# Kernel optimization log

Measured on AMD Instinct MI355X. Metric: run time of the kernel, lower is better.

The kernel has to match this reference:

```python
import jax, jax.numpy as jnp
import numpy as np

N = 50000
E = 800000
IN_C = 128
HID = 128
OUT_C = 128
EPS = 1e-5


def _glorot(key, shape):
    fan_in = shape[-1]
    return jax.random.normal(key, shape, dtype=jnp.float32) / jnp.sqrt(jnp.float32(fan_in))


def setup_inputs() -> dict:
    key = jax.random.key(0)
    ks = jax.random.split(key, 16)
    inp = {
        'x': jax.random.normal(ks[0], (N, IN_C), dtype=jnp.float32),
        'edge_index': jax.random.randint(ks[1], (2, E), 0, N, dtype=jnp.int64),
    }
    dims = [(IN_C, HID), (HID, HID), (HID, OUT_C)]
    for i, (din, dout) in enumerate(dims, start=1):
        inp[f'Wl{i}'] = _glorot(ks[2 * i], (dout, din))      # applied to aggregated neighbors
        inp[f'bl{i}'] = jnp.zeros((dout,), dtype=jnp.float32)
        inp[f'Wr{i}'] = _glorot(ks[2 * i + 1], (dout, din))  # applied to root node
        inp[f'g{i}'] = jnp.ones((dout,), dtype=jnp.float32)   # BN gamma
        inp[f'b{i}'] = jnp.zeros((dout,), dtype=jnp.float32)  # BN beta
    inp['Wlin'] = _glorot(ks[10], (OUT_C, 2 * HID + OUT_C))
    inp['blin'] = jnp.zeros((OUT_C,), dtype=jnp.float32)
    return inp


def _sage(x, src, dst, Wl, bl, Wr):
    # mean aggregation of source features at target nodes (PyG SAGEConv default)
    msg = x[src]                                              # [E, C]
    s = jax.ops.segment_sum(msg, dst, num_segments=N)         # [N, C]
    cnt = jax.ops.segment_sum(jnp.ones((src.shape[0], 1), x.dtype), dst, num_segments=N)
    aggr = s / jnp.maximum(cnt, 1.0)
    return aggr @ Wl.T + bl + x @ Wr.T


def _bn(x, g, b):
    # training-mode BatchNorm1d over the node dimension
    mu = jnp.mean(x, axis=0)
    var = jnp.var(x, axis=0)
    return g * (x - mu) * jax.lax.rsqrt(var + EPS) + b


def reference(x, edge_index, Wl1, bl1, Wr1, g1, b1, Wl2, bl2, Wr2, g2, b2,
              Wl3, bl3, Wr3, g3, b3, Wlin, blin):
    src, dst = edge_index[0], edge_index[1]
    x1 = _bn(jax.nn.relu(_sage(x, src, dst, Wl1, bl1, Wr1)), g1, b1)
    x2 = _bn(jax.nn.relu(_sage(x1, src, dst, Wl2, bl2, Wr2)), g2, b2)
    x3 = _bn(jax.nn.relu(_sage(x2, src, dst, Wl3, bl3, Wr3)), g3, b3)
    cat = jnp.concatenate([x1, x2, x3], axis=-1)              # [N, 2*HID + OUT_C]
    return jax.nn.relu(cat @ Wlin.T + blin)
```

## Files before the change

### kernel.cpp

```cpp
#include <hip/hip_runtime.h>

#define NN 50000
#define NE 800000
#define CH 128
#define EPSV 1e-5f
#define NPASS 2
#define PRANGE 25000
#define NBLK 49

typedef unsigned short ushort_t;
typedef __attribute__((ext_vector_type(8))) short short8_t;
typedef __attribute__((ext_vector_type(8))) unsigned short u16x8;
typedef __attribute__((ext_vector_type(4))) float f32x4;

#define AS1 __attribute__((address_space(1)))
#define AS3 __attribute__((address_space(3)))

__device__ inline float bf2f(ushort_t u) {
    union { unsigned int i; float f; } t; t.i = ((unsigned int)u) << 16; return t.f;
}
__device__ inline ushort_t f2bf(float f) {
    union { float f; unsigned int i; } t; t.f = f;
    unsigned int r = t.i + 0x7fff + ((t.i >> 16) & 1);
    return (ushort_t)(r >> 16);
}


__global__ void k_hist(const int* __restrict__ dst, int* __restrict__ deg) {
    int e = blockIdx.x * 256 + threadIdx.x;
    if (e < NE) atomicAdd(&deg[dst[e]], 1);
}

__global__ __launch_bounds__(1024) void k_scanA(const int* __restrict__ deg,
                                                int* __restrict__ rp,
                                                int* __restrict__ btot) {
    __shared__ int wsum[16];
    const int t = threadIdx.x;
    const int lane = t & 63;
    const int wid = t >> 6;
    const int i = blockIdx.x * 1024 + t;
    int v = (i < NN) ? deg[i] : 0;
    int x = v;
    #pragma unroll
    for (int off = 1; off < 64; off <<= 1) {
        int y = __shfl_up(x, off, 64);
        if (lane >= off) x += y;
    }
    if (lane == 63) wsum[wid] = x;
    __syncthreads();
    if (wid == 0 && lane < 16) {
        int s = wsum[lane];
        #pragma unroll
        for (int off = 1; off < 16; off <<= 1) {
            int y = __shfl_up(s, off, 16);
            if (lane >= off) s += y;
        }
        wsum[lane] = s;
    }
    __syncthreads();
    int wbase = (wid > 0) ? wsum[wid - 1] : 0;
    if (i < NN) rp[i] = wbase + x - v;
    if (wid == 15 && lane == 63) btot[blockIdx.x] = wbase + x;
}

__global__ void k_scanB(const int* __restrict__ btot, int* __restrict__ boffs,
                        int* __restrict__ rp) {
    int t = threadIdx.x;
    int v = (t < NBLK) ? btot[t] : 0;
    int x = v;
    #pragma unroll
    for (int off = 1; off < 64; off <<= 1) {
        int y = __shfl_up(x, off, 64);
        if (t >= off) x += y;
    }
    if (t < NBLK) boffs[t] = x - v;
    if (t == NBLK - 1) rp[NN] = x;
}

__global__ __launch_bounds__(256) void k_scanC(int* __restrict__ rp,
                                               const int* __restrict__ boffs) {
    int i = blockIdx.x * 256 + threadIdx.x;
    if (i < NN) rp[i] += boffs[i >> 10];
}

__global__ void k_fillp(const int* __restrict__ src, const int* __restrict__ dst,
                        const int* __restrict__ rp, int* __restrict__ cur,
                        int* __restrict__ csr, int lo, int hi) {
    int e = blockIdx.x * 256 + threadIdx.x;
    if (e < NE) {
        int d = dst[e];
        int s = src[e];
        if (d >= lo && d < hi) {
            int pos = rp[d] + atomicAdd(&cur[d], 1);
            csr[pos] = s;
        }
    }
}


__global__ __launch_bounds__(256) void k_cvtpack(const float* __restrict__ x,
        ushort_t* __restrict__ xb, const float* __restrict__ s0,
        const float* __restrict__ s1, ushort_t* __restrict__ Wp1,
        float* __restrict__ bn_sums) {
    if (blockIdx.x < 6250) {
        int i = blockIdx.x * 256 + threadIdx.x;
        if (blockIdx.x == 0) {
            bn_sums[threadIdx.x] = 0.f;
            bn_sums[256 + threadIdx.x] = 0.f;
            bn_sums[512 + threadIdx.x] = 0.f;
        }
        if (i >= NN * 32) return;
        float4 v = ((const float4*)x)[i];
        ushort4 o;
        o.x = f2bf(v.x); o.y = f2bf(v.y); o.z = f2bf(v.z); o.w = f2bf(v.w);
        ((ushort4*)xb)[i] = o;
    } else {
        int t = (blockIdx.x - 6250) * 256 + threadIdx.x;
        int o = t >> 8, k = t & 255;
        float v = (k < 128) ? s0[o * 128 + k] : s1[o * 128 + k - 128];
        Wp1[t] = f2bf(v);
    }
}

__global__ void k_foldnext(const float* __restrict__ bn_sums,
                           const float* __restrict__ g, const float* __restrict__ b,
                           const float* __restrict__ Wl, const float* __restrict__ Wr,
                           const float* __restrict__ bl,
                           ushort_t* __restrict__ Wp, float* __restrict__ bias,
                           float* __restrict__ abg) {
    __shared__ float red[128];
    int o = blockIdx.x;
    int k = threadIdx.x;
    float mu = bn_sums[k] * (1.0f / NN);
    float var = bn_sums[128 + k] * (1.0f / NN) - mu * mu;
    var = var > 0.f ? var : 0.f;
    float a = g[k] * rsqrtf(var + EPSV);
    float c = b[k] - a * mu;
    if (o == 0) { abg[k] = a; abg[128 + k] = c; }
    float wr = Wr[o * 128 + k];
    Wp[o * 256 + k]       = f2bf(Wl[o * 128 + k]);
    Wp[o * 256 + 128 + k] = f2bf(wr * a);
    red[k] = wr * c;
    __syncthreads();
    for (int s = 64; s > 0; s >>= 1) {
        if (k < s) red[k] += red[k + s];
        __syncthreads();
    }
    if (k == 0) bias[o] = bl[o] + red[0];
}

__global__ void k_foldF(const float* __restrict__ bn3,
                        const float* __restrict__ g3, const float* __restrict__ b3,
                        const float* __restrict__ ab1, const float* __restrict__ ab2,
                        const float* __restrict__ Wlin, const float* __restrict__ blin,
                        ushort_t* __restrict__ Wp, float* __restrict__ bias) {
    __shared__ float red[128];
    int o = blockIdx.x;
    int k = threadIdx.x;
    float mu = bn3[k] * (1.0f / NN);
    float var = bn3[128 + k] * (1.0f / NN) - mu * mu;
    var = var > 0.f ? var : 0.f;
    float a3 = g3[k] * rsqrtf(var + EPSV);
    float c3 = b3[k] - a3 * mu;
    float w1 = Wlin[o * 384 + k];
    float w2 = Wlin[o * 384 + 128 + k];
    float w3 = Wlin[o * 384 + 256 + k];
    Wp[o * 384 + k]       = f2bf(w1 * ab1[k]);
    Wp[o * 384 + 128 + k] = f2bf(w2 * ab2[k]);
    Wp[o * 384 + 256 + k] = f2bf(w3 * a3);
    red[k] = w1 * ab1[128 + k] + w2 * ab2[128 + k] + w3 * c3;
    __syncthreads();
    for (int s = 64; s > 0; s >>= 1) {
        if (k < s) red[k] += red[k + s];
        __syncthreads();
    }
    if (k == 0) bias[o] = blin[o] + red[0];
}


template<bool FOLD>
__global__ __launch_bounds__(256) void k_aggr(const ushort_t* __restrict__ x,
        const int* __restrict__ rp, const int* __restrict__ csr,
        const float* __restrict__ ab, ushort_t* __restrict__ aggr) {
    const int node = blockIdx.x * 4 + (threadIdx.x >> 6);
    const int lane = threadIdx.x & 63;
    const int l4 = lane & 15;
    const int q  = lane >> 4;
    const int r0 = rp[node], r1 = rp[node + 1];
    const int d = r1 - r0;
    const ushort_t* xrow = x + l4 * 8;

    float accA[8] = {0, 0, 0, 0, 0, 0, 0, 0};
    float accB[8] = {0, 0, 0, 0, 0, 0, 0, 0};

    int j = r0 + q;
    for (; j + 12 < r1; j += 16) {
        int s0 = csr[j], s1 = csr[j + 4], s2 = csr[j + 8], s3 = csr[j + 12];
        u16x8 v0 = *(const u16x8*)(xrow + (size_t)s0 * CH);
        u16x8 v1 = *(const u16x8*)(xrow + (size_t)s1 * CH);
        u16x8 v2 = *(const u16x8*)(xrow + (size_t)s2 * CH);
        u16x8 v3 = *(const u16x8*)(xrow + (size_t)s3 * CH);
        #pragma unroll
        for (int i = 0; i < 8; ++i) {
            accA[i] += bf2f(v0[i]) + bf2f(v1[i]);
            accB[i] += bf2f(v2[i]) + bf2f(v3[i]);
        }
    }
    for (; j < r1; j += 4) {
        int s0 = csr[j];
        u16x8 v0 = *(const u16x8*)(xrow + (size_t)s0 * CH);
        #pragma unroll
        for (int i = 0; i < 8; ++i) accA[i] += bf2f(v0[i]);
    }

    const float sc = d > 0 ? 1.0f / (float)d : 0.0f;
    #pragma unroll
    for (int i = 0; i < 8; ++i) {
        float s = accA[i] + accB[i];
        s += __shfl_xor(s, 16);
        s += __shfl_xor(s, 32);
        accA[i] = s * sc;
    }

    if (q == 0) {
        u16x8 ov;
        #pragma unroll
        for (int i = 0; i < 8; ++i) {
            float v = accA[i];
            if (FOLD) v = d > 0 ? fmaf(v, ab[l4 * 8 + i], ab[128 + l4 * 8 + i]) : 0.f;
            ov[i] = f2bf(v);
        }
        *(u16x8*)&aggr[(size_t)node * CH + l4 * 8] = ov;
    }
}


#define STAGE(buf, t) do {                                                           \
    const ushort_t* Ab_ = (((t) >> 1) == 0) ? A0 : ((((t) >> 1) == 1) ? A1 : A2);    \
    Ab_ += ((t) & 1) * 64;                                                           \
    const ushort_t* Wb_ = W + (t) * 64;                                              \
    _Pragma("unroll")                                                                \
    for (int i_ = 0; i_ < 4; ++i_) {                                                 \
        int f_ = i_ * 256 + tid;                                                     \
        int row_ = f_ >> 3;                                                          \
        int c_ = (f_ & 7) ^ (row_ & 7);                                              \
        int gr_ = bn0 + row_; gr_ = gr_ < NN ? gr_ : NN - 1;                         \
        __builtin_amdgcn_global_load_lds(                                            \
            (const AS1 unsigned int*)(Ab_ + (size_t)gr_ * CH + c_ * 8),              \
            (AS3 unsigned int*)(&Abuf[buf][f_ * 8]), 16, 0, 0);                      \
        __builtin_amdgcn_global_load_lds(                                            \
            (const AS1 unsigned int*)(Wb_ + (size_t)row_ * (NT * 64) + c_ * 8),      \
            (AS3 unsigned int*)(&Wbuf[buf][f_ * 8]), 16, 0, 0);                      \
    } } while (0)

template<int NT, bool STATS, bool F32OUT>
__global__ __launch_bounds__(256, 2) void k_mgemm(
    const ushort_t* __restrict__ A0, const ushort_t* __restrict__ A1,
    const ushort_t* __restrict__ A2,
    const ushort_t* __restrict__ W, const float* __restrict__ bias,
    ushort_t* __restrict__ outb, float* __restrict__ outf,
    float* __restrict__ bn_sums)
{
    __shared__ __align__(16) ushort_t Abuf[2][128 * 64];
    __shared__ __align__(16) ushort_t Wbuf[2][128 * 64];
    __shared__ float bns[128], bnq[128];

    const int tid  = threadIdx.x;
    const int lane = tid & 63;
    const int wid  = tid >> 6;
    const int l15  = lane & 15;
    const int lg   = lane >> 4;
    const int wn   = (wid >> 1) * 64;
    const int wo   = (wid & 1) * 64;
    const int bn0  = blockIdx.x * 128;

    if (STATS && tid < 128) { bns[tid] = 0.f; bnq[tid] = 0.f; }

    f32x4 acc[4][4];
    #pragma unroll
    for (int i = 0; i < 4; ++i)
        #pragma unroll
        for (int j = 0; j < 4; ++j)
            acc[i][j] = (f32x4){0.f, 0.f, 0.f, 0.f};

    STAGE(0, 0);
    asm volatile("s_waitcnt vmcnt(0)");
    __syncthreads();

    #pragma unroll
    for (int t = 0; t < NT; ++t) {
        const int cur = t & 1;
        if (t + 1 < NT) STAGE(cur ^ 1, t + 1);
        #pragma unroll
        for (int s = 0; s < 2; ++s) {
            short8_t af[4], wf[4];
            #pragma unroll
            for (int b = 0; b < 4; ++b) {
                int ra = wn + b * 16 + l15;
                int ca = (s * 4 + lg) ^ (ra & 7);
                af[b] = *(const short8_t*)&Abuf[cur][ra * 64 + ca * 8];
                int rw = wo + b * 16 + l15;
                int cw = (s * 4 + lg) ^ (rw & 7);
                wf[b] = *(const short8_t*)&Wbuf[cur][rw * 64 + cw * 8];
            }
            #pragma unroll
            for (int i = 0; i < 4; ++i)
                #pragma unroll
                for (int j = 0; j < 4; ++j)
                    acc[i][j] = __builtin_amdgcn_mfma_f32_16x16x32_bf16(
                        af[i], wf[j], acc[i][j], 0, 0, 0);
        }
        asm volatile("s_waitcnt vmcnt(0)");
        __syncthreads();
    }

    float bv[4];
    #pragma unroll
    for (int j = 0; j < 4; ++j) bv[j] = bias[wo + j * 16 + l15];

    float sum[4] = {0.f, 0.f, 0.f, 0.f}, sq[4] = {0.f, 0.f, 0.f, 0.f};

    #pragma unroll
    for (int i = 0; i < 4; ++i) {
        #pragma unroll
        for (int r = 0; r < 4; ++r) {
            int gn = bn0 + wn + i * 16 + lg * 4 + r;
            bool ok = gn < NN;
            #pragma unroll
            for (int j = 0; j < 4; ++j) {
                int o = wo + j * 16 + l15;
                float v = acc[i][j][r] + bv[j];
                v = fmaxf(v, 0.f);
                if (ok) {
                    if (F32OUT) outf[(size_t)gn * CH + o] = v;
                    else        outb[(size_t)gn * CH + o] = f2bf(v);
                    if (STATS) { sum[j] += v; sq[j] += v * v; }
                }
            }
        }
    }

    if (STATS) {
        #pragma unroll
        for (int j = 0; j < 4; ++j) {
            float ss = sum[j], qq = sq[j];
            ss += __shfl_xor(ss, 16); qq += __shfl_xor(qq, 16);
            ss += __shfl_xor(ss, 32); qq += __shfl_xor(qq, 32);
            if (lg == 0) {
                atomicAdd(&bns[wo + j * 16 + l15], ss);
                atomicAdd(&bnq[wo + j * 16 + l15], qq);
            }
        }
        __syncthreads();
        if (tid < 128) {
            atomicAdd(&bn_sums[tid], bns[tid]);
            atomicAdd(&bn_sums[128 + tid], bnq[tid]);
        }
    }
}


extern "C" void kernel_launch(void* const* d_in, const int* in_sizes, int n_in,
                              void* d_out, int out_size, void* d_ws, size_t ws_size,
                              hipStream_t stream) {
    const float* x  = (const float*)d_in[0];
    const int*   ei = (const int*)d_in[1];
    const int* esrc = ei;
    const int* edst = ei + NE;

    const float* Wl[3] = {(const float*)d_in[2],  (const float*)d_in[7],  (const float*)d_in[12]};
    const float* bl[3] = {(const float*)d_in[3],  (const float*)d_in[8],  (const float*)d_in[13]};
    const float* Wr[3] = {(const float*)d_in[4],  (const float*)d_in[9],  (const float*)d_in[14]};
    const float* gg[3] = {(const float*)d_in[5],  (const float*)d_in[10], (const float*)d_in[15]};
    const float* bb[3] = {(const float*)d_in[6],  (const float*)d_in[11], (const float*)d_in[16]};
    const float* Wlin  = (const float*)d_in[17];
    const float* blin  = (const float*)d_in[18];

    float* fo = (float*)d_out;

    const size_t NC = (size_t)NN * CH;
    ushort_t* xb     = (ushort_t*)d_ws;
    ushort_t* y1b    = xb + NC;
    ushort_t* y2b    = y1b + NC;
    ushort_t* y3b    = y2b + NC;
    ushort_t* aggr_b = y3b + NC;
    ushort_t* Wp1    = aggr_b + NC;
    ushort_t* Wp2    = Wp1 + 128 * 256;
    ushort_t* Wp3    = Wp2 + 128 * 256;
    ushort_t* WpF    = Wp3 + 128 * 256;
    float* bias2     = (float*)(WpF + 128 * 384);
    float* bias3     = bias2 + 128;
    float* biasF     = bias3 + 128;
    float* bn_sums   = biasF + 128;
    float* ab        = bn_sums + 768;
    int* btot        = (int*)(ab + 512);
    int* boffs       = btot + 64;
    int* deg         = boffs + 64;
    int* cur         = deg + NN;
    int* rp          = cur + NN;
    int* csr         = rp + NN + 1;

    hipMemsetAsync(deg, 0, 2 * NN * sizeof(int), stream);
    k_hist<<<(NE + 255) / 256, 256, 0, stream>>>(edst, deg);
    k_scanA<<<NBLK, 1024, 0, stream>>>(deg, rp, btot);
    k_scanB<<<1, 64, 0, stream>>>(btot, boffs, rp);
    k_scanC<<<(NN + 255) / 256, 256, 0, stream>>>(rp, boffs);
    for (int p = 0; p < NPASS; ++p)
        k_fillp<<<NE / 256, 256, 0, stream>>>(esrc, edst, rp, cur, csr,
                                              p * PRANGE, (p + 1) * PRANGE);

    k_cvtpack<<<6250 + 128, 256, 0, stream>>>(x, xb, Wl[0], Wr[0], Wp1, bn_sums);

    const int GEMM_GRID = (NN + 127) / 128;
    const int AGGR_GRID = NN / 4;

    k_aggr<false><<<AGGR_GRID, 256, 0, stream>>>(xb, rp, csr, nullptr, aggr_b);
    k_mgemm<4, true, false><<<GEMM_GRID, 256, 0, stream>>>(
        aggr_b, xb, nullptr, Wp1, bl[0], y1b, nullptr, bn_sums);
    k_foldnext<<<128, 128, 0, stream>>>(bn_sums, gg[0], bb[0],
                                        Wl[1], Wr[1], bl[1], Wp2, bias2, ab);

    k_aggr<true><<<AGGR_GRID, 256, 0, stream>>>(y1b, rp, csr, ab, aggr_b);
    k_mgemm<4, true, false><<<GEMM_GRID, 256, 0, stream>>>(
        aggr_b, y1b, nullptr, Wp2, bias2, y2b, nullptr, bn_sums + 256);
    k_foldnext<<<128, 128, 0, stream>>>(bn_sums + 256, gg[1], bb[1],
                                        Wl[2], Wr[2], bl[2], Wp3, bias3, ab + 256);

    k_aggr<true><<<AGGR_GRID, 256, 0, stream>>>(y2b, rp, csr, ab + 256, aggr_b);
    k_mgemm<4, true, false><<<GEMM_GRID, 256, 0, stream>>>(
        aggr_b, y2b, nullptr, Wp3, bias3, y3b, nullptr, bn_sums + 512);
    k_foldF<<<128, 128, 0, stream>>>(bn_sums + 512, gg[2], bb[2], ab, ab + 256,
                                     Wlin, blin, WpF, biasF);

    k_mgemm<6, false, true><<<GEMM_GRID, 256, 0, stream>>>(
        y1b, y2b, y3b, WpF, biasF, nullptr, fo, nullptr);
}
```

Baseline: 318.8 us.

## Quantize node features to int8 for neighbor gather-aggregation

Neighbor aggregation now gathers int8-quantized feature rows instead of bf16, halving gather bytes, and accumulates in integers before rescaling by per-channel scales. Input scales come from a new column-max kernel. Hidden-layer scales come from BN statistics (mean plus 8 std), applied by a new requant kernel after each GEMM. This adds extra kernels and passes, and clamps outliers beyond the heuristic range, which loses accuracy. y3b is aliased onto the xq buffer to save workspace.

```diff
diff --git a/kernel.cpp b/kernel.cpp
--- a/kernel.cpp
+++ b/kernel.cpp
@@ -98,10 +98,23 @@
 }
 
 
+__global__ __launch_bounds__(256) void k_xmax(const float* __restrict__ x,
+                                              unsigned* __restrict__ gmax) {
+    int t = blockIdx.x * 256 + threadIdx.x;
+    int c = t & 127;
+    float m = 0.f;
+    for (int r = t >> 7; r < NN; r += 512)
+        m = fmaxf(m, fabsf(x[(size_t)r * CH + c]));
+    atomicMax(&gmax[c], __float_as_uint(m));
+}
+
+
 __global__ __launch_bounds__(256) void k_cvtpack(const float* __restrict__ x,
-        ushort_t* __restrict__ xb, const float* __restrict__ s0,
-        const float* __restrict__ s1, ushort_t* __restrict__ Wp1,
-        float* __restrict__ bn_sums) {
+        ushort_t* __restrict__ xb, signed char* __restrict__ xq,
+        const unsigned* __restrict__ gmax,
+        const float* __restrict__ s0, const float* __restrict__ s1,
+        ushort_t* __restrict__ Wp1, float* __restrict__ bn_sums,
+        float* __restrict__ sdx) {
     if (blockIdx.x < 6250) {
         int i = blockIdx.x * 256 + threadIdx.x;
         if (blockIdx.x == 0) {
@@ -114,11 +127,26 @@
         ushort4 o;
         o.x = f2bf(v.x); o.y = f2bf(v.y); o.z = f2bf(v.z); o.w = f2bf(v.w);
         ((ushort4*)xb)[i] = o;
-    } else {
+        int c0 = (i * 4) & 127;
+        unsigned pk = 0;
+        float vv[4] = {v.x, v.y, v.z, v.w};
+        #pragma unroll
+        for (int k = 0; k < 4; ++k) {
+            float g = __uint_as_float(gmax[c0 + k]);
+            float inv = g > 1e-20f ? 127.0f / g : 0.f;
+            int qv = __float2int_rn(vv[k] * inv);
+            qv = qv > 127 ? 127 : (qv < -127 ? -127 : qv);
+            pk |= ((unsigned)(qv & 0xFF)) << (8 * k);
+        }
+        ((unsigned*)xq)[i] = pk;
+    } else if (blockIdx.x < 6250 + 128) {
         int t = (blockIdx.x - 6250) * 256 + threadIdx.x;
         int o = t >> 8, k = t & 255;
         float v = (k < 128) ? s0[o * 128 + k] : s1[o * 128 + k - 128];
         Wp1[t] = f2bf(v);
+    } else {
+        if (threadIdx.x < 128)
+            sdx[threadIdx.x] = __uint_as_float(gmax[threadIdx.x]) * (1.0f / 127.0f);
     }
 }
 
@@ -127,7 +155,8 @@
                            const float* __restrict__ Wl, const float* __restrict__ Wr,
                            const float* __restrict__ bl,
                            ushort_t* __restrict__ Wp, float* __restrict__ bias,
-                           float* __restrict__ abg) {
+                           float* __restrict__ abg, float* __restrict__ sdec,
+                           float* __restrict__ sinvv) {
     __shared__ float red[128];
     int o = blockIdx.x;
     int k = threadIdx.x;
@@ -136,7 +165,12 @@
     var = var > 0.f ? var : 0.f;
     float a = g[k] * rsqrtf(var + EPSV);
     float c = b[k] - a * mu;
-    if (o == 0) { abg[k] = a; abg[128 + k] = c; }
+    if (o == 0) {
+        abg[k] = a; abg[128 + k] = c;
+        float vm = mu + 8.0f * sqrtf(var);
+        sdec[k]  = vm * (1.0f / 127.0f);
+        sinvv[k] = vm > 1e-10f ? 127.0f / vm : 0.f;
+    }
     float wr = Wr[o * 128 + k];
     Wp[o * 256 + k]       = f2bf(Wl[o * 128 + k]);
     Wp[o * 256 + 128 + k] = f2bf(wr * a);
@@ -178,55 +212,86 @@
 }
 
 
+__global__ __launch_bounds__(256) void k_requant(const ushort_t* __restrict__ y,
+        const float* __restrict__ sinvv, signed char* __restrict__ qout) {
+    int i = blockIdx.x * 256 + threadIdx.x;
+    if (i >= NN * 16) return;
+    u16x8 v = *(const u16x8*)&y[(size_t)i * 8];
+    int c0 = (i * 8) & 127;
+    unsigned lo = 0, hi = 0;
+    #pragma unroll
+    for (int k = 0; k < 8; ++k) {
+        int qv = __float2int_rn(bf2f(v[k]) * sinvv[c0 + k]);
+        qv = qv > 127 ? 127 : qv;
+        if (k < 4) lo |= ((unsigned)(qv & 0xFF)) << (8 * k);
+        else       hi |= ((unsigned)(qv & 0xFF)) << (8 * (k - 4));
+    }
+    ((uint2*)qout)[i] = make_uint2(lo, hi);
+}
+
+
+#define ACCI(acc, w) do {                                                  \
+    unsigned a0_ = (w).x, a1_ = (w).y;                                     \
+    acc[0] += (int)(signed char)(a0_);                                     \
+    acc[1] += (int)(signed char)(a0_ >> 8);                                \
+    acc[2] += (int)(signed char)(a0_ >> 16);                               \
+    acc[3] += (int)(signed char)(a0_ >> 24);                               \
+    acc[4] += (int)(signed char)(a1_);                                     \
+    acc[5] += (int)(signed char)(a1_ >> 8);                                \
+    acc[6] += (int)(signed char)(a1_ >> 16);                               \
+    acc[7] += (int)(signed char)(a1_ >> 24);                               \
+} while (0)
+
 template<bool FOLD>
-__global__ __launch_bounds__(256) void k_aggr(const ushort_t* __restrict__ x,
+__global__ __launch_bounds__(256) void k_aggr8(const signed char* __restrict__ xq,
         const int* __restrict__ rp, const int* __restrict__ csr,
-        const float* __restrict__ ab, ushort_t* __restrict__ aggr) {
+        const float* __restrict__ sd, const float* __restrict__ ab,
+        ushort_t* __restrict__ aggr) {
     const int node = blockIdx.x * 4 + (threadIdx.x >> 6);
     const int lane = threadIdx.x & 63;
     const int l4 = lane & 15;
     const int q  = lane >> 4;
     const int r0 = rp[node], r1 = rp[node + 1];
     const int d = r1 - r0;
-    const ushort_t* xrow = x + l4 * 8;
-
-    float accA[8] = {0, 0, 0, 0, 0, 0, 0, 0};
-    float accB[8] = {0, 0, 0, 0, 0, 0, 0, 0};
+    const signed char* xrow = xq + l4 * 8;
+
+    float sd8[8];
+    #pragma unroll
+    for (int i = 0; i < 8; ++i) sd8[i] = sd[l4 * 8 + i];
+
+    int accA[8] = {0, 0, 0, 0, 0, 0, 0, 0};
+    int accB[8] = {0, 0, 0, 0, 0, 0, 0, 0};
 
     int j = r0 + q;
     for (; j + 12 < r1; j += 16) {
         int s0 = csr[j], s1 = csr[j + 4], s2 = csr[j + 8], s3 = csr[j + 12];
-        u16x8 v0 = *(const u16x8*)(xrow + (size_t)s0 * CH);
-        u16x8 v1 = *(const u16x8*)(xrow + (size_t)s1 * CH);
-        u16x8 v2 = *(const u16x8*)(xrow + (size_t)s2 * CH);
-        u16x8 v3 = *(const u16x8*)(xrow + (size_t)s3 * CH);
-        #pragma unroll
-        for (int i = 0; i < 8; ++i) {
-            accA[i] += bf2f(v0[i]) + bf2f(v1[i]);
-            accB[i] += bf2f(v2[i]) + bf2f(v3[i]);
-        }
+        uint2 w0 = *(const uint2*)(xrow + (size_t)s0 * CH);
+        uint2 w1 = *(const uint2*)(xrow + (size_t)s1 * CH);
+        uint2 w2 = *(const uint2*)(xrow + (size_t)s2 * CH);
+        uint2 w3 = *(const uint2*)(xrow + (size_t)s3 * CH);
+        ACCI(accA, w0); ACCI(accA, w1);
+        ACCI(accB, w2); ACCI(accB, w3);
     }
     for (; j < r1; j += 4) {
-        int s0 = csr[j];
-        u16x8 v0 = *(const u16x8*)(xrow + (size_t)s0 * CH);
-        #pragma unroll
-        for (int i = 0; i < 8; ++i) accA[i] += bf2f(v0[i]);
-    }
-
-    const float sc = d > 0 ? 1.0f / (float)d : 0.0f;
+        uint2 w0 = *(const uint2*)(xrow + (size_t)csr[j] * CH);
+        ACCI(accA, w0);
+    }
+
+    const float scdeg = d > 0 ? 1.0f / (float)d : 0.0f;
+    float af[8];
     #pragma unroll
     for (int i = 0; i < 8; ++i) {
-        float s = accA[i] + accB[i];
+        int s = accA[i] + accB[i];
         s += __shfl_xor(s, 16);
         s += __shfl_xor(s, 32);
-        accA[i] = s * sc;
+        af[i] = (float)s * sd8[i] * scdeg;
     }
 
     if (q == 0) {
         u16x8 ov;
         #pragma unroll
         for (int i = 0; i < 8; ++i) {
-            float v = accA[i];
+            float v = af[i];
             if (FOLD) v = d > 0 ? fmaf(v, ab[l4 * 8 + i], ab[128 + l4 * 8 + i]) : 0.f;
             ov[i] = f2bf(v);
         }
@@ -379,28 +444,37 @@
     float* fo = (float*)d_out;
 
     const size_t NC = (size_t)NN * CH;
-    ushort_t* xb     = (ushort_t*)d_ws;
-    ushort_t* y1b    = xb + NC;
-    ushort_t* y2b    = y1b + NC;
-    ushort_t* y3b    = y2b + NC;
-    ushort_t* aggr_b = y3b + NC;
-    ushort_t* Wp1    = aggr_b + NC;
-    ushort_t* Wp2    = Wp1 + 128 * 256;
-    ushort_t* Wp3    = Wp2 + 128 * 256;
-    ushort_t* WpF    = Wp3 + 128 * 256;
-    float* bias2     = (float*)(WpF + 128 * 384);
-    float* bias3     = bias2 + 128;
-    float* biasF     = bias3 + 128;
-    float* bn_sums   = biasF + 128;
-    float* ab        = bn_sums + 768;
-    int* btot        = (int*)(ab + 512);
-    int* boffs       = btot + 64;
-    int* deg         = boffs + 64;
-    int* cur         = deg + NN;
-    int* rp          = cur + NN;
-    int* csr         = rp + NN + 1;
-
-    hipMemsetAsync(deg, 0, 2 * NN * sizeof(int), stream);
+    ushort_t* xb       = (ushort_t*)d_ws;
+    ushort_t* y1b      = xb + NC;
+    ushort_t* y2b      = y1b + NC;
+    ushort_t* aggr_b   = y2b + NC;
+    signed char* xq    = (signed char*)(aggr_b + NC);
+    signed char* y1q   = xq + NC;
+    ushort_t* y3b      = (ushort_t*)xq;
+    signed char* y2q   = y1q + NC;
+    ushort_t* Wp1      = (ushort_t*)(y2q + NC);
+    ushort_t* Wp2      = Wp1 + 128 * 256;
+    ushort_t* Wp3      = Wp2 + 128 * 256;
+    ushort_t* WpF      = Wp3 + 128 * 256;
+    float* bias2       = (float*)(WpF + 128 * 384);
+    float* bias3       = bias2 + 128;
+    float* biasF       = bias3 + 128;
+    float* bn_sums     = biasF + 128;
+    float* ab          = bn_sums + 768;
+    float* sdx         = ab + 512;
+    float* sd1         = sdx + 128;
+    float* sinv1       = sd1 + 128;
+    float* sd2         = sinv1 + 128;
+    float* sinv2       = sd2 + 128;
+    int* btot          = (int*)(sinv2 + 128);
+    int* boffs         = btot + 64;
+    int* deg           = boffs + 64;
+    int* cur           = deg + NN;
+    unsigned* gmax     = (unsigned*)(cur + NN);
+    int* rp            = (int*)(gmax + 128);
+    int* csr           = rp + NN + 1;
+
+    hipMemsetAsync(deg, 0, (2 * NN + 128) * sizeof(int), stream);
     k_hist<<<(NE + 255) / 256, 256, 0, stream>>>(edst, deg);
     k_scanA<<<NBLK, 1024, 0, stream>>>(deg, rp, btot);
     k_scanB<<<1, 64, 0, stream>>>(btot, boffs, rp);
@@ -409,24 +483,29 @@
         k_fillp<<<NE / 256, 256, 0, stream>>>(esrc, edst, rp, cur, csr,
                                               p * PRANGE, (p + 1) * PRANGE);
 
-    k_cvtpack<<<6250 + 128, 256, 0, stream>>>(x, xb, Wl[0], Wr[0], Wp1, bn_sums);
+    k_xmax<<<256, 256, 0, stream>>>(x, gmax);
+    k_cvtpack<<<6250 + 128 + 1, 256, 0, stream>>>(x, xb, xq, gmax,
+                                                  Wl[0], Wr[0], Wp1, bn_sums, sdx);
 
     const int GEMM_GRID = (NN + 127) / 128;
     const int AGGR_GRID = NN / 4;
-
-    k_aggr<false><<<AGGR_GRID, 256, 0, stream>>>(xb, rp, csr, nullptr, aggr_b);
+    const int RQ_GRID   = (NN * 16 + 255) / 256;
+
+    k_aggr8<false><<<AGGR_GRID, 256, 0, stream>>>(xq, rp, csr, sdx, nullptr, aggr_b);
     k_mgemm<4, true, false><<<GEMM_GRID, 256, 0, stream>>>(
         aggr_b, xb, nullptr, Wp1, bl[0], y1b, nullptr, bn_sums);
     k_foldnext<<<128, 128, 0, stream>>>(bn_sums, gg[0], bb[0],
-                                        Wl[1], Wr[1], bl[1], Wp2, bias2, ab);
-
-    k_aggr<true><<<AGGR_GRID, 256, 0, stream>>>(y1b, rp, csr, ab, aggr_b);
+                                        Wl[1], Wr[1], bl[1], Wp2, bias2, ab, sd1, sinv1);
+    k_requant<<<RQ_GRID, 256, 0, stream>>>(y1b, sinv1, y1q);
+
+    k_aggr8<true><<<AGGR_GRID, 256, 0, stream>>>(y1q, rp, csr, sd1, ab, aggr_b);
     k_mgemm<4, true, false><<<GEMM_GRID, 256, 0, stream>>>(
         aggr_b, y1b, nullptr, Wp2, bias2, y2b, nullptr, bn_sums + 256);
     k_foldnext<<<128, 128, 0, stream>>>(bn_sums + 256, gg[1], bb[1],
-                                        Wl[2], Wr[2], bl[2], Wp3, bias3, ab + 256);
-
-    k_aggr<true><<<AGGR_GRID, 256, 0, stream>>>(y2b, rp, csr, ab + 256, aggr_b);
+                                        Wl[2], Wr[2], bl[2], Wp3, bias3, ab + 256, sd2, sinv2);
+    k_requant<<<RQ_GRID, 256, 0, stream>>>(y2b, sinv2, y2q);
+
+    k_aggr8<true><<<AGGR_GRID, 256, 0, stream>>>(y2q, rp, csr, sd2, ab + 256, aggr_b);
     k_mgemm<4, true, false><<<GEMM_GRID, 256, 0, stream>>>(
         aggr_b, y2b, nullptr, Wp3, bias3, y3b, nullptr, bn_sums + 512);
     k_foldF<<<128, 128, 0, stream>>>(bn_sums + 512, gg[2], bb[2], ab, ab + 256,
```

New measurement: 346.0 us, median of 4. +8.5%, slower.
